# Performance work log

Measured on AMD Instinct MI355X. Metric: run time of the kernel, lower is better.

The kernel has to match this reference:

```python
import jax, jax.numpy as jnp
import numpy as np

B, S, DIM, H, D = 4, 2048, 1024, 16, 64
WINDOW = 512  # max_mem_segments * window_size


def _rotary_angles(seq_len, dim_head):
    inv_freq = 1.0 / (10000.0 ** (jnp.arange(0, dim_head, 2, dtype=jnp.float32) / dim_head))
    freqs = jnp.arange(seq_len, dtype=jnp.float32)[:, None] * inv_freq[None, :]  # [S, D/2]
    return jnp.repeat(freqs, 2, axis=-1)  # [S, D] interleaved


def _rotate_half(x):
    x1 = x[..., 0::2]
    x2 = x[..., 1::2]
    return jnp.stack((-x2, x1), axis=-1).reshape(x.shape)


def _apply_rotary(x, angles):
    # x: [b h n d], angles: [n d]
    return x * jnp.cos(angles) + _rotate_half(x) * jnp.sin(angles)


def setup_inputs() -> dict:
    key = jax.random.key(0)
    ks = jax.random.split(key, 7)
    tokens = jax.random.normal(ks[0], (B, S, DIM), dtype=jnp.float32)
    value_residual = jax.random.normal(ks[1], (B, H, S, D), dtype=jnp.float32)
    s = 0.02
    Wq = jax.random.normal(ks[2], (DIM, H * D), dtype=jnp.float32) * s
    Wkv = jax.random.normal(ks[3], (DIM, 2 * H * D), dtype=jnp.float32) * s
    Wout = jax.random.normal(ks[4], (H * D, DIM), dtype=jnp.float32) * s
    Wgate = jax.random.normal(ks[5], (DIM, H), dtype=jnp.float32) * s
    Wmix = jax.random.normal(ks[6], (DIM, H), dtype=jnp.float32) * s
    return {"tokens": tokens, "value_residual": value_residual, "Wq": Wq,
            "Wkv": Wkv, "Wout": Wout, "Wgate": Wgate, "Wmix": Wmix}


def reference(tokens, value_residual, Wq, Wkv, Wout, Wgate, Wmix):
    b, n, dim = tokens.shape
    scale = D ** -0.5

    def split_heads(t):  # [b n (h d)] -> [b h n d]
        return t.reshape(b, n, H, D).transpose(0, 2, 1, 3)

    q = split_heads(tokens @ Wq)
    kv = tokens @ Wkv
    k = split_heads(kv[..., : H * D])
    v = split_heads(kv[..., H * D:])

    q = q * scale

    # value-residual lerp: v.lerp(value_residual, mix)
    mix = jax.nn.sigmoid(jnp.einsum('bnd,dh->bhn', tokens, Wmix))[..., None]  # [b h n 1]
    v = v + (value_residual - v) * mix

    angles = _rotary_angles(n, D)
    q = _apply_rotary(q, angles)
    k = _apply_rotary(k, angles)

    sim = jnp.einsum('bhid,bhjd->bhij', q, k)

    # fixed-window causal mask: dist = i - j; masked if dist < 0 or dist > WINDOW
    pos = jnp.arange(n)
    dist = pos[:, None] - pos[None, :]
    mask = (dist < 0) | (dist > WINDOW)
    neg = -jnp.finfo(sim.dtype).max
    sim = jnp.where(mask[None, None], neg, sim)

    attn = jax.nn.softmax(sim, axis=-1)
    out = jnp.einsum('bhij,bhjd->bhid', attn, v)

    gates = jax.nn.sigmoid(jnp.einsum('bnd,dh->bhn', tokens, Wgate))[..., None]  # [b h n 1]
    out = out * gates

    out = out.transpose(0, 2, 1, 3).reshape(b, n, H * D)
    return out @ Wout
```

## Files before the change

### kernel.cpp

```cpp
#include <hip/hip_runtime.h>

#define NH 16
#define SLEN 2048
#define DMODEL 1024
#define DHEAD 64
#define WIN 512
#define NB 4

typedef unsigned short u16;
typedef unsigned int u32;
typedef unsigned long long u64;
typedef __attribute__((ext_vector_type(8))) __bf16 bf16x8;
typedef __attribute__((ext_vector_type(4))) float floatx4;

__device__ __forceinline__ float b2f(u32 bits16) {
  union { u32 i; float f; } x; x.i = bits16 << 16; return x.f;
}
__device__ __forceinline__ u16 f2b(float f) {
  union { float f; u32 i; } x; x.f = f;
  u32 r = x.i + 0x7fffu + ((x.i >> 16) & 1u);
  return (u16)(r >> 16);
}

__device__ __forceinline__ void gl2lds16(const u16* g, u16* l) {
  __builtin_amdgcn_global_load_lds(
      (const __attribute__((address_space(1))) unsigned int*)g,
      (__attribute__((address_space(3))) unsigned int*)l, 16, 0, 0);
}

__global__ __launch_bounds__(256) void prep_all(
    const float* __restrict__ tokens, const float* __restrict__ Wq,
    const float* __restrict__ Wkv, const float* __restrict__ Wout,
    const float* __restrict__ Wmix, const float* __restrict__ Wgate,
    u64* __restrict__ tokA64, u16* __restrict__ WqkvT, u16* __restrict__ WoutT,
    u16* __restrict__ Wmg, float2* __restrict__ rtab) {
  __shared__ u16 T[64][72];
  const int blk = blockIdx.x, tid = threadIdx.x;
  if (blk < 8192) {
    int i = blk * 256 + tid;
    float4 f = reinterpret_cast<const float4*>(tokens)[i];
    union { u16 u[4]; u64 ll; } pk;
    pk.u[0] = f2b(f.x); pk.u[1] = f2b(f.y); pk.u[2] = f2b(f.z); pk.u[3] = f2b(f.w);
    tokA64[i] = pk.ll;
  } else if (blk < 9216) {
    const float* src; u16* dst; int ld, nb, n0, k0;
    if (blk < 8960) {
      int tile = blk - 8192;
      n0 = (tile % 48) * 64; k0 = (tile / 48) * 64;
      if (n0 < 1024) { src = Wq; ld = 1024; nb = n0; }
      else { src = Wkv; ld = 2048; nb = n0 - 1024; }
      dst = WqkvT;
    } else {
      int tile = blk - 8960;
      n0 = (tile % 16) * 64; k0 = (tile / 16) * 64;
      src = Wout; ld = 1024; nb = n0; dst = WoutT;
    }
#pragma unroll
    for (int i = 0; i < 16; ++i) {
      int e = i * 256 + tid;
      int kr = e >> 6, nc = e & 63;
      T[kr][nc] = f2b(src[(size_t)(k0 + kr) * ld + nb + nc]);
    }
    __syncthreads();
#pragma unroll
    for (int i = 0; i < 16; ++i) {
      int e = i * 256 + tid;
      int nr = e >> 6, kc = e & 63;
      dst[(size_t)(n0 + nr) * 1024 + k0 + kc] = T[kc][nr];
    }
  } else if (blk < 9344) {
    int idx = (blk - 9216) * 256 + tid;
    int n = idx >> 10, k = idx & 1023;
    float v = (n < 16) ? Wmix[k * 16 + n] : Wgate[k * 16 + (n - 16)];
    Wmg[idx] = f2b(v);
  } else {
    int idx = (blk - 9344) * 256 + tid;
    int s = idx >> 5, t = idx & 31;
    float inv = __expf((float)t * -0.2878231366f);
    float ang = (float)s * inv;
    float sn, cs;
    __sincosf(ang, &sn, &cs);
    rtab[idx] = make_float2(cs, sn);
  }
}

__global__ __launch_bounds__(256) void mixgate_mfma(const u16* __restrict__ A,
    const u16* __restrict__ Wmg, float* __restrict__ mixws, float* __restrict__ gatews) {
  const int lane = threadIdx.x & 63, w = threadIdx.x >> 6;
  const int lm = lane & 15, quad = lane >> 4;
  const int row0 = (blockIdx.x * 4 + w) * 32;

  floatx4 acc[2][2];
#pragma unroll
  for (int i = 0; i < 2; ++i)
#pragma unroll
    for (int j = 0; j < 2; ++j)
      acc[i][j] = (floatx4){0.f, 0.f, 0.f, 0.f};

#pragma unroll 4
  for (int k0 = 0; k0 < 1024; k0 += 32) {
    bf16x8 af[2], bf[2];
#pragma unroll
    for (int mt = 0; mt < 2; ++mt)
      af[mt] = *reinterpret_cast<const bf16x8*>(
          &A[(size_t)(row0 + mt * 16 + lm) * 1024 + k0 + quad * 8]);
#pragma unroll
    for (int nt = 0; nt < 2; ++nt)
      bf[nt] = *reinterpret_cast<const bf16x8*>(
          &Wmg[(size_t)(nt * 16 + lm) * 1024 + k0 + quad * 8]);
#pragma unroll
    for (int mt = 0; mt < 2; ++mt)
#pragma unroll
      for (int nt = 0; nt < 2; ++nt)
        acc[mt][nt] = __builtin_amdgcn_mfma_f32_16x16x32_bf16(af[mt], bf[nt], acc[mt][nt], 0, 0, 0);
  }

#pragma unroll
  for (int mt = 0; mt < 2; ++mt)
#pragma unroll
    for (int r = 0; r < 4; ++r) {
      int grow = row0 + mt * 16 + quad * 4 + r;
      int b = grow >> 11, s = grow & 2047;
#pragma unroll
      for (int nt = 0; nt < 2; ++nt) {
        int n = nt * 16 + lm;
        float sig = 1.0f / (1.0f + __expf(-acc[mt][nt][r]));
        int h = n & 15;
        (n < 16 ? mixws : gatews)[(b * NH + h) * SLEN + s] = sig;
      }
    }
}

template<int MODE>
__global__ __launch_bounds__(256, 3) void gemm_bf16_bt(
    const u16* __restrict__ A, const u16* __restrict__ Bt,
    float* __restrict__ C,
    u16* __restrict__ qws, u16* __restrict__ kws, u16* __restrict__ vws,
    const float* __restrict__ vres, const float* __restrict__ mixws,
    const float2* __restrict__ rtab,
    int M, int N, int K) {
  __shared__ u16 smem[16384];
  u16* As = smem;
  u16* Bs = smem + 8192;
  const int tid = threadIdx.x;
  const int row0 = blockIdx.y * 128, col0 = blockIdx.x * 128;
  const int w = tid >> 6, lane = tid & 63;
  const int wr = (w >> 1) * 64, wc = (w & 1) * 64;
  const int lm = lane & 15, quad = lane >> 4;

  floatx4 acc[4][4];
#pragma unroll
  for (int i = 0; i < 4; ++i)
#pragma unroll
    for (int j = 0; j < 4; ++j)
      acc[i][j] = (floatx4){0.f, 0.f, 0.f, 0.f};

  for (int k0 = 0; k0 < K; k0 += 64) {
#pragma unroll
    for (int i = 0; i < 4; ++i) {
      int slot = i * 256 + tid;
      int r = slot >> 3, cc = slot & 7;
      int csrc = (cc ^ (r & 7)) * 8;
      gl2lds16(&A[(size_t)(row0 + r) * K + k0 + csrc], As + slot * 8);
      gl2lds16(&Bt[(size_t)(col0 + r) * K + k0 + csrc], Bs + slot * 8);
    }
    __syncthreads();
#pragma unroll
    for (int j = 0; j < 2; ++j) {
      bf16x8 af[4], bfr[4];
#pragma unroll
      for (int mt = 0; mt < 4; ++mt) {
        int ra = wr + mt * 16 + lm;
        af[mt] = *reinterpret_cast<const bf16x8*>(As + (ra * 8 + ((j * 4 + quad) ^ (ra & 7))) * 8);
      }
#pragma unroll
      for (int nt = 0; nt < 4; ++nt) {
        int rb = wc + nt * 16 + lm;
        bfr[nt] = *reinterpret_cast<const bf16x8*>(Bs + (rb * 8 + ((j * 4 + quad) ^ (rb & 7))) * 8);
      }
#pragma unroll
      for (int mt = 0; mt < 4; ++mt)
#pragma unroll
        for (int nt = 0; nt < 4; ++nt)
          acc[mt][nt] = __builtin_amdgcn_mfma_f32_16x16x32_bf16(af[mt], bfr[nt], acc[mt][nt], 0, 0, 0);
    }
    __syncthreads();
  }

  if (MODE == 0) {
#pragma unroll
    for (int mt = 0; mt < 4; ++mt)
#pragma unroll
      for (int r = 0; r < 4; ++r) {
        int grow = row0 + wr + mt * 16 + quad * 4 + r;
#pragma unroll
        for (int nt = 0; nt < 4; ++nt)
          C[(size_t)grow * N + col0 + wc + nt * 16 + lm] = acc[mt][nt][r];
      }
  } else {
    const int seg = col0 >> 10;
    const int b = row0 >> 11, s0 = row0 & 2047;
    if (seg < 2) {
      u16* dst = seg ? kws : qws;
      const float qs = seg ? 1.0f : 0.125f;
#pragma unroll
      for (int mt = 0; mt < 4; ++mt)
#pragma unroll
        for (int r = 0; r < 4; ++r) {
          int s = s0 + wr + mt * 16 + quad * 4 + r;
#pragma unroll
          for (int nt = 0; nt < 4; ++nt) {
            int nn = ((col0 + wc) & 1023) + nt * 16 + lm;
            int h = nn >> 6, d = nn & 63;
            float val = acc[mt][nt][r] * qs;
            float2 cs = rtab[(s << 5) + (d >> 1)];
            float partner = __shfl_xor(val, 1);
            float o = (d & 1) ? fmaf(val, cs.x, partner * cs.y)
                              : fmaf(val, cs.x, -partner * cs.y);
            dst[((size_t)((b * NH + h) * SLEN + s)) * 64 + d] = f2b(o);
          }
        }
    } else {
      const int h0 = (col0 - 2048) >> 6;
      u16 (*Vt)[136] = (u16(*)[136])smem;
#pragma unroll
      for (int p = 0; p < 2; ++p) {
        const int bh = b * NH + h0 + p;
        __syncthreads();
        if ((w & 1) == p) {
#pragma unroll
          for (int mt = 0; mt < 4; ++mt)
#pragma unroll
            for (int nt = 0; nt < 4; ++nt) {
              const int d = nt * 16 + lm;
              const int sl = wr + mt * 16 + quad * 4;
              union { u16 u[4]; u64 ll; } pk;
#pragma unroll
              for (int r = 0; r < 4; ++r) {
                int s = s0 + sl + r;
                float val = acc[mt][nt][r];
                float mv = mixws[bh * SLEN + s];
                float o = val + (vres[((size_t)(bh * SLEN + s)) * 64 + d] - val) * mv;
                pk.u[r] = f2b(o);
              }
              *reinterpret_cast<u64*>(&Vt[d][sl]) = pk.ll;
            }
        }
        __syncthreads();
        const int drow = tid >> 2, chunk = tid & 3;
        const u16* src = &Vt[drow][chunk * 32];
        u16* dst = vws + ((size_t)(bh * 64 + drow)) * SLEN + s0 + chunk * 32;
#pragma unroll
        for (int j = 0; j < 4; ++j)
          reinterpret_cast<uint4*>(dst)[j] = reinterpret_cast<const uint4*>(src)[j];
      }
    }
  }
}

__global__ __launch_bounds__(256) void attn_mfma_kernel(
    const u16* __restrict__ q, const u16* __restrict__ k, const u16* __restrict__ vt,
    const float* __restrict__ gate, u16* __restrict__ X) {
  __shared__ u16 Ks[4096];
  __shared__ u16 Vs[4096];
  __shared__ u16 Ps[4][16][72];
  const int tid = threadIdx.x;
  const int w = tid >> 6, lane = tid & 63;
  const int lm = lane & 15, quad = lane >> 4;
  const int blk = blockIdx.x;
  const int qt = blk & 31;
  const int h = (blk >> 5) & 15;
  const int b = blk >> 9;
  const int bh = b * NH + h;
  const int q0 = qt * 64;
  const size_t kqbase = (size_t)bh * SLEN * 64;
  const size_t vbase  = (size_t)bh * 64 * SLEN;

  bf16x8 qf[2];
  {
    const u16* qrow = q + kqbase + (size_t)(q0 + w * 16 + lm) * 64;
    qf[0] = *reinterpret_cast<const bf16x8*>(qrow + quad * 8);
    qf[1] = *reinterpret_cast<const bf16x8*>(qrow + 32 + quad * 8);
  }

  floatx4 o[4];
#pragma unroll
  for (int nt = 0; nt < 4; ++nt) o[nt] = (floatx4){0.f, 0.f, 0.f, 0.f};
  float lsum = 0.f;
  const int iq = q0 + w * 16 + lm;

  const int c_first = (q0 >= WIN) ? ((q0 - WIN) >> 6) : 0;
  const int c_last = q0 >> 6;
  const int vrow = tid >> 3, vcol = (tid & 7) * 8;
  for (int c = c_first; c <= c_last; ++c) {
    const int c0 = c << 6;
    __syncthreads();
    {
      const u16* kg = k + kqbase + (size_t)c0 * 64;
      gl2lds16(kg + tid * 8, Ks + tid * 8);
      gl2lds16(kg + 2048 + tid * 8, Ks + 2048 + tid * 8);
      const u16* vg = vt + vbase + c0;
      gl2lds16(vg + (size_t)vrow * SLEN + vcol, Vs + tid * 8);
      gl2lds16(vg + (size_t)(vrow + 32) * SLEN + vcol, Vs + 2048 + tid * 8);
    }
    __syncthreads();

    floatx4 st[4];
#pragma unroll
    for (int mt = 0; mt < 4; ++mt) {
      bf16x8 kf0 = *reinterpret_cast<const bf16x8*>(&Ks[(mt * 16 + lm) * 64 + quad * 8]);
      bf16x8 kf1 = *reinterpret_cast<const bf16x8*>(&Ks[(mt * 16 + lm) * 64 + 32 + quad * 8]);
      st[mt] = __builtin_amdgcn_mfma_f32_16x16x32_bf16(kf0, qf[0],
                   (floatx4){0.f, 0.f, 0.f, 0.f}, 0, 0, 0);
      st[mt] = __builtin_amdgcn_mfma_f32_16x16x32_bf16(kf1, qf[1], st[mt], 0, 0, 0);
    }
    const bool need_mask = (c == c_first && q0 >= WIN) || (c == c_last);
    if (need_mask) {
#pragma unroll
      for (int mt = 0; mt < 4; ++mt)
#pragma unroll
        for (int r = 0; r < 4; ++r) {
          int j = c0 + mt * 16 + quad * 4 + r;
          bool valid = (j <= iq) && (j >= iq - WIN);
          if (!valid) st[mt][r] = -3.0e38f;
        }
    }
    float p[4][4], psum = 0.f;
#pragma unroll
    for (int mt = 0; mt < 4; ++mt)
#pragma unroll
      for (int r = 0; r < 4; ++r) {
        p[mt][r] = __expf(st[mt][r]);
        psum += p[mt][r];
      }
    psum += __shfl_xor(psum, 16);
    psum += __shfl_xor(psum, 32);
    lsum += psum;
#pragma unroll
    for (int mt = 0; mt < 4; ++mt) {
      union { u16 u[4]; u64 ll; } pk;
#pragma unroll
      for (int r = 0; r < 4; ++r) pk.u[r] = f2b(p[mt][r]);
      *reinterpret_cast<u64*>(&Ps[w][lm][mt * 16 + quad * 4]) = pk.ll;
    }
    __builtin_amdgcn_wave_barrier();
    __builtin_amdgcn_s_waitcnt(0xC07F);
    __builtin_amdgcn_wave_barrier();
    bf16x8 af0 = *reinterpret_cast<const bf16x8*>(&Ps[w][lm][quad * 8]);
    bf16x8 af1 = *reinterpret_cast<const bf16x8*>(&Ps[w][lm][32 + quad * 8]);
#pragma unroll
    for (int nt = 0; nt < 4; ++nt) {
      bf16x8 vf0 = *reinterpret_cast<const bf16x8*>(&Vs[(nt * 16 + lm) * 64 + quad * 8]);
      bf16x8 vf1 = *reinterpret_cast<const bf16x8*>(&Vs[(nt * 16 + lm) * 64 + 32 + quad * 8]);
      o[nt] = __builtin_amdgcn_mfma_f32_16x16x32_bf16(af0, vf0, o[nt], 0, 0, 0);
      o[nt] = __builtin_amdgcn_mfma_f32_16x16x32_bf16(af1, vf1, o[nt], 0, 0, 0);
    }
  }
  float linv[4], g[4];
#pragma unroll
  for (int r = 0; r < 4; ++r) {
    linv[r] = 1.0f / __shfl(lsum, quad * 4 + r);
    g[r] = gate[bh * SLEN + q0 + w * 16 + quad * 4 + r];
  }
#pragma unroll
  for (int r = 0; r < 4; ++r) {
    int i = q0 + w * 16 + quad * 4 + r;
    u16* xrow = X + ((size_t)(b * SLEN + i)) * 1024 + h * 64;
#pragma unroll
    for (int nt = 0; nt < 4; ++nt)
      xrow[nt * 16 + lm] = f2b(o[nt][r] * linv[r] * g[r]);
  }
}

extern "C" void kernel_launch(void* const* d_in, const int* in_sizes, int n_in,
                              void* d_out, int out_size, void* d_ws, size_t ws_size,
                              hipStream_t stream) {
  (void)in_sizes; (void)n_in; (void)out_size; (void)ws_size;
  const float* tokens = (const float*)d_in[0];
  const float* vres   = (const float*)d_in[1];
  const float* Wq     = (const float*)d_in[2];
  const float* Wkv    = (const float*)d_in[3];
  const float* Wout   = (const float*)d_in[4];
  const float* Wgate  = (const float*)d_in[5];
  const float* Wmix   = (const float*)d_in[6];
  float* out = (float*)d_out;

  char* p = (char*)d_ws;
  auto alloc = [&](size_t bytes) { char* r = p; p += (bytes + 255) & ~(size_t)255; return r; };
  u16*  tokA   = (u16*)alloc(8192ull * 1024 * 2);
  u16*  WqkvT  = (u16*)alloc(3072ull * 1024 * 2);
  u16*  WoutT  = (u16*)alloc(1024ull * 1024 * 2);
  u16*  Wmg    = (u16*)alloc(32ull * 1024 * 2);
  float2* rtab = (float2*)alloc(65536ull * 8);
  u16*  qws    = (u16*)alloc(8388608ull * 2);
  u16*  kws    = (u16*)alloc(8388608ull * 2);
  u16*  vws    = (u16*)alloc(8388608ull * 2);
  u16*  Xws    = (u16*)alloc(8388608ull * 2);
  float* mixws = (float*)alloc(131072ull * 4);
  float* gatews= (float*)alloc(131072ull * 4);

  prep_all<<<9600, 256, 0, stream>>>(tokens, Wq, Wkv, Wout, Wmix, Wgate,
      (u64*)tokA, WqkvT, WoutT, Wmg, rtab);
  mixgate_mfma<<<64, 256, 0, stream>>>(tokA, Wmg, mixws, gatews);
  gemm_bf16_bt<1><<<dim3(24, 64), 256, 0, stream>>>(tokA, WqkvT, nullptr,
      qws, kws, vws, vres, mixws, rtab, 8192, 3072, 1024);
  attn_mfma_kernel<<<2048, 256, 0, stream>>>(qws, kws, vws, gatews, Xws);
  gemm_bf16_bt<0><<<dim3(8, 64), 256, 0, stream>>>(Xws, WoutT, out,
      nullptr, nullptr, nullptr, nullptr, nullptr, nullptr, 8192, 1024, 1024);
}
```

Before: 298.1 us.

## Rewrite GEMM as 256x128-tile triple-buffered pipeline with 512 threads and swizzled block order

Replaces the single-buffered 128x128 GEMM with a 256x128 tile computed by 512 threads. A three-stage LDS ring issues global-to-LDS loads two k-steps ahead, interleaved between MFMA halves, with explicit vmcnt waits, a single barrier per step, and s_setprio around the MFMA blocks. Work-group ids are remapped in groups of eight to improve L2 locality, and the V-transpose epilogue now handles both heads at once. The aim is to hide global load latency and cut barrier stalls, at the cost of much more LDS per block and lower occupancy.

```diff
diff --git a/kernel.cpp b/kernel.cpp
--- a/kernel.cpp
+++ b/kernel.cpp
@@ -132,21 +132,23 @@
 }
 
 template<int MODE>
-__global__ __launch_bounds__(256, 3) void gemm_bf16_bt(
+__global__ __launch_bounds__(512, 2) void gemm_pipe(
     const u16* __restrict__ A, const u16* __restrict__ Bt,
     float* __restrict__ C,
     u16* __restrict__ qws, u16* __restrict__ kws, u16* __restrict__ vws,
     const float* __restrict__ vres, const float* __restrict__ mixws,
-    const float2* __restrict__ rtab,
-    int M, int N, int K) {
-  __shared__ u16 smem[16384];
-  u16* As = smem;
-  u16* Bs = smem + 8192;
+    const float2* __restrict__ rtab, int N) {
+  __shared__ u16 smem[73728];
   const int tid = threadIdx.x;
-  const int row0 = blockIdx.y * 128, col0 = blockIdx.x * 128;
+  const int nbx = N >> 7;
+  const int wg = (blockIdx.x & 7) * (gridDim.x >> 3) + (blockIdx.x >> 3);
+  const int bx = wg % nbx, by = wg / nbx;
+  const int row0 = by * 256, col0 = bx * 128;
   const int w = tid >> 6, lane = tid & 63;
   const int wr = (w >> 1) * 64, wc = (w & 1) * 64;
   const int lm = lane & 15, quad = lane >> 4;
+  const int NT = 16;
+  const int sr = tid >> 3, sc = tid & 7;
 
   floatx4 acc[4][4];
 #pragma unroll
@@ -155,36 +157,116 @@
     for (int j = 0; j < 4; ++j)
       acc[i][j] = (floatx4){0.f, 0.f, 0.f, 0.f};
 
-  for (int k0 = 0; k0 < K; k0 += 64) {
-#pragma unroll
-    for (int i = 0; i < 4; ++i) {
-      int slot = i * 256 + tid;
-      int r = slot >> 3, cc = slot & 7;
-      int csrc = (cc ^ (r & 7)) * 8;
-      gl2lds16(&A[(size_t)(row0 + r) * K + k0 + csrc], As + slot * 8);
-      gl2lds16(&Bt[(size_t)(col0 + r) * K + k0 + csrc], Bs + slot * 8);
-    }
-    __syncthreads();
-#pragma unroll
-    for (int j = 0; j < 2; ++j) {
-      bf16x8 af[4], bfr[4];
-#pragma unroll
-      for (int mt = 0; mt < 4; ++mt) {
-        int ra = wr + mt * 16 + lm;
-        af[mt] = *reinterpret_cast<const bf16x8*>(As + (ra * 8 + ((j * 4 + quad) ^ (ra & 7))) * 8);
-      }
-#pragma unroll
-      for (int nt = 0; nt < 4; ++nt) {
-        int rb = wc + nt * 16 + lm;
-        bfr[nt] = *reinterpret_cast<const bf16x8*>(Bs + (rb * 8 + ((j * 4 + quad) ^ (rb & 7))) * 8);
-      }
-#pragma unroll
-      for (int mt = 0; mt < 4; ++mt)
-#pragma unroll
-        for (int nt = 0; nt < 4; ++nt)
-          acc[mt][nt] = __builtin_amdgcn_mfma_f32_16x16x32_bf16(af[mt], bfr[nt], acc[mt][nt], 0, 0, 0);
-    }
-    __syncthreads();
+#pragma unroll
+  for (int tt = 0; tt < 2; ++tt) {
+    u16* As = smem + tt * 24576;
+    u16* Bs = As + 16384;
+    const int k0 = tt * 64;
+#pragma unroll
+    for (int la = 0; la < 4; ++la) {
+      int r = la * 64 + sr;
+      gl2lds16(&A[(size_t)(row0 + r) * 1024 + k0 + ((sc ^ (r & 7)) << 3)],
+               As + (((r << 3) + sc) << 3));
+    }
+#pragma unroll
+    for (int lb = 0; lb < 2; ++lb) {
+      int r = lb * 64 + sr;
+      gl2lds16(&Bt[(size_t)(col0 + r) * 1024 + k0 + ((sc ^ (r & 7)) << 3)],
+               Bs + (((r << 3) + sc) << 3));
+    }
+  }
+
+  int cur = 0;
+  for (int t = 0; t < NT; ++t) {
+    u16* As = smem + cur * 24576;
+    u16* Bs = As + 16384;
+    if (t < NT - 1) { asm volatile("s_waitcnt vmcnt(6)" ::: "memory"); }
+    else           { asm volatile("s_waitcnt vmcnt(0)" ::: "memory"); }
+    __builtin_amdgcn_s_barrier();
+    asm volatile("" ::: "memory");
+
+    int sidx = cur + 2; if (sidx >= 3) sidx -= 3;
+    u16* Sa = smem + sidx * 24576;
+    u16* Sb = Sa + 16384;
+    const int ks = (t + 2) << 6;
+    const bool do_stage = (t + 2) < NT;
+
+    if (do_stage) {
+#pragma unroll
+      for (int la = 0; la < 2; ++la) {
+        int r = la * 64 + sr;
+        gl2lds16(&A[(size_t)(row0 + r) * 1024 + ks + ((sc ^ (r & 7)) << 3)],
+                 Sa + (((r << 3) + sc) << 3));
+      }
+      {
+        int r = sr;
+        gl2lds16(&Bt[(size_t)(col0 + r) * 1024 + ks + ((sc ^ (r & 7)) << 3)],
+                 Sb + (((r << 3) + sc) << 3));
+      }
+    }
+    bf16x8 bfr[4][2];
+#pragma unroll
+    for (int nt = 0; nt < 4; ++nt) {
+      int rb = wc + nt * 16 + lm;
+#pragma unroll
+      for (int j = 0; j < 2; ++j)
+        bfr[nt][j] = *reinterpret_cast<const bf16x8*>(
+            Bs + (((rb << 3) + (((j << 2) + quad) ^ (rb & 7))) << 3));
+    }
+    bf16x8 af0[2][2];
+#pragma unroll
+    for (int mh = 0; mh < 2; ++mh) {
+      int ra = wr + mh * 16 + lm;
+#pragma unroll
+      for (int j = 0; j < 2; ++j)
+        af0[mh][j] = *reinterpret_cast<const bf16x8*>(
+            As + (((ra << 3) + (((j << 2) + quad) ^ (ra & 7))) << 3));
+    }
+    __builtin_amdgcn_s_setprio(1);
+#pragma unroll
+    for (int mh = 0; mh < 2; ++mh)
+#pragma unroll
+      for (int nt = 0; nt < 4; ++nt)
+#pragma unroll
+        for (int j = 0; j < 2; ++j)
+          acc[mh][nt] = __builtin_amdgcn_mfma_f32_16x16x32_bf16(
+              af0[mh][j], bfr[nt][j], acc[mh][nt], 0, 0, 0);
+    __builtin_amdgcn_s_setprio(0);
+
+    if (do_stage) {
+#pragma unroll
+      for (int la = 2; la < 4; ++la) {
+        int r = la * 64 + sr;
+        gl2lds16(&A[(size_t)(row0 + r) * 1024 + ks + ((sc ^ (r & 7)) << 3)],
+                 Sa + (((r << 3) + sc) << 3));
+      }
+      {
+        int r = 64 + sr;
+        gl2lds16(&Bt[(size_t)(col0 + r) * 1024 + ks + ((sc ^ (r & 7)) << 3)],
+                 Sb + (((r << 3) + sc) << 3));
+      }
+    }
+    bf16x8 af1[2][2];
+#pragma unroll
+    for (int mh = 0; mh < 2; ++mh) {
+      int ra = wr + (2 + mh) * 16 + lm;
+#pragma unroll
+      for (int j = 0; j < 2; ++j)
+        af1[mh][j] = *reinterpret_cast<const bf16x8*>(
+            As + (((ra << 3) + (((j << 2) + quad) ^ (ra & 7))) << 3));
+    }
+    __builtin_amdgcn_s_setprio(1);
+#pragma unroll
+    for (int mh = 0; mh < 2; ++mh)
+#pragma unroll
+      for (int nt = 0; nt < 4; ++nt)
+#pragma unroll
+        for (int j = 0; j < 2; ++j)
+          acc[2 + mh][nt] = __builtin_amdgcn_mfma_f32_16x16x32_bf16(
+              af1[mh][j], bfr[nt][j], acc[2 + mh][nt], 0, 0, 0);
+    __builtin_amdgcn_s_setprio(0);
+
+    cur += 1; if (cur >= 3) cur -= 3;
   }
 
   if (MODE == 0) {
@@ -199,18 +281,19 @@
       }
   } else {
     const int seg = col0 >> 10;
-    const int b = row0 >> 11, s0 = row0 & 2047;
     if (seg < 2) {
       u16* dst = seg ? kws : qws;
       const float qs = seg ? 1.0f : 0.125f;
+      const int colb = (col0 & 1023) + wc;
 #pragma unroll
       for (int mt = 0; mt < 4; ++mt)
 #pragma unroll
         for (int r = 0; r < 4; ++r) {
-          int s = s0 + wr + mt * 16 + quad * 4 + r;
+          int sg = row0 + wr + mt * 16 + quad * 4 + r;
+          int b = sg >> 11, s = sg & 2047;
 #pragma unroll
           for (int nt = 0; nt < 4; ++nt) {
-            int nn = ((col0 + wc) & 1023) + nt * 16 + lm;
+            int nn = colb + nt * 16 + lm;
             int h = nn >> 6, d = nn & 63;
             float val = acc[mt][nt][r] * qs;
             float2 cs = rtab[(s << 5) + (d >> 1)];
@@ -222,37 +305,37 @@
         }
     } else {
       const int h0 = (col0 - 2048) >> 6;
-      u16 (*Vt)[136] = (u16(*)[136])smem;
-#pragma unroll
-      for (int p = 0; p < 2; ++p) {
-        const int bh = b * NH + h0 + p;
-        __syncthreads();
-        if ((w & 1) == p) {
-#pragma unroll
-          for (int mt = 0; mt < 4; ++mt)
-#pragma unroll
-            for (int nt = 0; nt < 4; ++nt) {
-              const int d = nt * 16 + lm;
-              const int sl = wr + mt * 16 + quad * 4;
-              union { u16 u[4]; u64 ll; } pk;
-#pragma unroll
-              for (int r = 0; r < 4; ++r) {
-                int s = s0 + sl + r;
-                float val = acc[mt][nt][r];
-                float mv = mixws[bh * SLEN + s];
-                float o = val + (vres[((size_t)(bh * SLEN + s)) * 64 + d] - val) * mv;
-                pk.u[r] = f2b(o);
-              }
-              *reinterpret_cast<u64*>(&Vt[d][sl]) = pk.ll;
-            }
+      const int p = (w & 1);
+      const int b = row0 >> 11, s0 = row0 & 2047;
+      const int bh = b * NH + h0 + p;
+      u16 (*Vt)[264] = reinterpret_cast<u16(*)[264]>(smem + p * 16896);
+      __syncthreads();
+#pragma unroll
+      for (int mt = 0; mt < 4; ++mt)
+#pragma unroll
+        for (int nt = 0; nt < 4; ++nt) {
+          const int d = nt * 16 + lm;
+          const int sl = wr + mt * 16 + quad * 4;
+          union { u16 u[4]; u64 ll; } pk;
+#pragma unroll
+          for (int r = 0; r < 4; ++r) {
+            int s = s0 + sl + r;
+            float val = acc[mt][nt][r];
+            float mv = mixws[bh * SLEN + s];
+            float o = val + (vres[((size_t)(bh * SLEN + s)) * 64 + d] - val) * mv;
+            pk.u[r] = f2b(o);
+          }
+          *reinterpret_cast<u64*>(&Vt[d][sl]) = pk.ll;
         }
-        __syncthreads();
-        const int drow = tid >> 2, chunk = tid & 3;
-        const u16* src = &Vt[drow][chunk * 32];
-        u16* dst = vws + ((size_t)(bh * 64 + drow)) * SLEN + s0 + chunk * 32;
-#pragma unroll
-        for (int j = 0; j < 4; ++j)
-          reinterpret_cast<uint4*>(dst)[j] = reinterpret_cast<const uint4*>(src)[j];
+      __syncthreads();
+#pragma unroll
+      for (int it = 0; it < 8; ++it) {
+        int idx = it * 512 + tid;
+        int ph = idx >> 11, rem = idx & 2047;
+        int d = rem >> 5, ch = rem & 31;
+        const u16* src = smem + ph * 16896 + d * 264 + ch * 8;
+        u16* dst = vws + ((size_t)((b * NH + h0 + ph) * 64 + d)) * SLEN + s0 + ch * 8;
+        *reinterpret_cast<uint4*>(dst) = *reinterpret_cast<const uint4*>(src);
       }
     }
   }
@@ -402,9 +485,9 @@
   prep_all<<<9600, 256, 0, stream>>>(tokens, Wq, Wkv, Wout, Wmix, Wgate,
       (u64*)tokA, WqkvT, WoutT, Wmg, rtab);
   mixgate_mfma<<<64, 256, 0, stream>>>(tokA, Wmg, mixws, gatews);
-  gemm_bf16_bt<1><<<dim3(24, 64), 256, 0, stream>>>(tokA, WqkvT, nullptr,
-      qws, kws, vws, vres, mixws, rtab, 8192, 3072, 1024);
+  gemm_pipe<1><<<768, 512, 0, stream>>>(tokA, WqkvT, nullptr,
+      qws, kws, vws, vres, mixws, rtab, 3072);
   attn_mfma_kernel<<<2048, 256, 0, stream>>>(qws, kws, vws, gatews, Xws);
-  gemm_bf16_bt<0><<<dim3(8, 64), 256, 0, stream>>>(Xws, WoutT, out,
-      nullptr, nullptr, nullptr, nullptr, nullptr, nullptr, 8192, 1024, 1024);
-}
+  gemm_pipe<0><<<256, 512, 0, stream>>>(Xws, WoutT, out,
+      nullptr, nullptr, nullptr, nullptr, nullptr, nullptr, 1024);
+}
```

New measurement: 286.0 us. 4.1% less time.

## Replace projection GEMMs with triple-buffered 256x128 pipelined kernel and swizzled grid

Applied to the files above, without the earlier changes.

Both projection GEMMs move to a new kernel with 512-thread blocks computing 256x128 tiles. It triple-buffers LDS stages so global-to-LDS loads run two K-steps ahead of the MFMA work, using explicit vmcnt waits, raw ds_read_b128 with immediate offsets, and setprio around the MFMA bursts. The grid is remapped into an XCD-friendly order to improve L2 reuse. The epilogue is adjusted for the taller tile, including a single-pass V transpose through LDS. The cost is much larger LDS use and hard-coded K=1024 and wait counts.

```diff
diff --git a/kernel.cpp b/kernel.cpp
--- a/kernel.cpp
+++ b/kernel.cpp
@@ -27,6 +27,20 @@
       (const __attribute__((address_space(1))) unsigned int*)g,
       (__attribute__((address_space(3))) unsigned int*)l, 16, 0, 0);
 }
+
+template<int OFF>
+__device__ __forceinline__ bf16x8 ldsr128(u32 addr) {
+  bf16x8 r;
+  if constexpr (OFF == 0)
+    asm volatile("ds_read_b128 %0, %1" : "=v"(r) : "v"(addr));
+  else
+    asm volatile("ds_read_b128 %0, %1 offset:%2" : "=v"(r) : "v"(addr), "i"(OFF));
+  return r;
+}
+
+#define WAIT_VM6  asm volatile("s_waitcnt vmcnt(6)" ::: "memory")
+#define WAIT_VM0  asm volatile("s_waitcnt vmcnt(0)" ::: "memory")
+#define WAIT_LGKM0 asm volatile("s_waitcnt lgkmcnt(0)" ::: "memory")
 
 __global__ __launch_bounds__(256) void prep_all(
     const float* __restrict__ tokens, const float* __restrict__ Wq,
@@ -132,21 +146,35 @@
 }
 
 template<int MODE>
-__global__ __launch_bounds__(256, 3) void gemm_bf16_bt(
+__global__ __launch_bounds__(512, 2) void gemm_pipe(
     const u16* __restrict__ A, const u16* __restrict__ Bt,
     float* __restrict__ C,
     u16* __restrict__ qws, u16* __restrict__ kws, u16* __restrict__ vws,
     const float* __restrict__ vres, const float* __restrict__ mixws,
-    const float2* __restrict__ rtab,
-    int M, int N, int K) {
-  __shared__ u16 smem[16384];
-  u16* As = smem;
-  u16* Bs = smem + 8192;
+    const float2* __restrict__ rtab, int N) {
+  __shared__ u16 smem[73728];
   const int tid = threadIdx.x;
-  const int row0 = blockIdx.y * 128, col0 = blockIdx.x * 128;
+  const int nbx = N >> 7;
+  const int wg = (blockIdx.x & 7) * (gridDim.x >> 3) + (blockIdx.x >> 3);
+  const int bx = wg % nbx, by = wg / nbx;
+  const int row0 = by * 256, col0 = bx * 128;
   const int w = tid >> 6, lane = tid & 63;
   const int wr = (w >> 1) * 64, wc = (w & 1) * 64;
   const int lm = lane & 15, quad = lane >> 4;
+  const int NT = 16;
+  const int sr = tid >> 3, sc = tid & 7;
+  const int sl0 = (sr * 8 + sc) * 8;
+  const u16* gA = A + (size_t)(row0 + sr) * 1024 + ((sc ^ (sr & 7)) << 3);
+  const u16* gB = Bt + (size_t)(col0 + sr) * 1024 + ((sc ^ (sr & 7)) << 3);
+
+  const u32 ldsbase = (u32)(size_t)(__attribute__((address_space(3))) u16*)smem;
+  u32 arow[2], brow[2];
+#pragma unroll
+  for (int j = 0; j < 2; ++j) {
+    u32 cslot = (u32)((j * 4 + quad) ^ (lm & 7));
+    arow[j] = (u32)(wr + lm) * 128 + cslot * 16;
+    brow[j] = (u32)(wc + lm) * 128 + cslot * 16;
+  }
 
   floatx4 acc[4][4];
 #pragma unroll
@@ -155,36 +183,67 @@
     for (int j = 0; j < 4; ++j)
       acc[i][j] = (floatx4){0.f, 0.f, 0.f, 0.f};
 
-  for (int k0 = 0; k0 < K; k0 += 64) {
-#pragma unroll
-    for (int i = 0; i < 4; ++i) {
-      int slot = i * 256 + tid;
-      int r = slot >> 3, cc = slot & 7;
-      int csrc = (cc ^ (r & 7)) * 8;
-      gl2lds16(&A[(size_t)(row0 + r) * K + k0 + csrc], As + slot * 8);
-      gl2lds16(&Bt[(size_t)(col0 + r) * K + k0 + csrc], Bs + slot * 8);
-    }
-    __syncthreads();
+  auto stage3 = [&](u16* Sa, u16* Sb, int ks, int half) {
+    if (half == 0) {
+      gl2lds16(gA + ks, Sa + sl0);
+      gl2lds16(gA + 65536 + ks, Sa + 4096 + sl0);
+      gl2lds16(gB + ks, Sb + sl0);
+    } else {
+      gl2lds16(gA + 131072 + ks, Sa + 8192 + sl0);
+      gl2lds16(gA + 196608 + ks, Sa + 12288 + sl0);
+      gl2lds16(gB + 65536 + ks, Sb + 4096 + sl0);
+    }
+  };
+
+#pragma unroll
+  for (int tt = 0; tt < 2; ++tt) {
+    u16* Sa = smem + tt * 24576;
+    u16* Sb = Sa + 16384;
+    stage3(Sa, Sb, tt * 64, 0);
+    stage3(Sa, Sb, tt * 64, 1);
+  }
+
+  int cur = 0;
+  for (int t = 0; t < NT; ++t) {
+    int sidx = cur + 2; if (sidx >= 3) sidx -= 3;
+    u16* Sa = smem + sidx * 24576;
+    u16* Sb = Sa + 16384;
+    const int ks = (t + 2) << 6;
+    const bool do_stage = t < NT - 2;
+    const u32 abase = ldsbase + (u32)cur * 49152u;
+
+    if (t < NT - 1) { WAIT_VM6; } else { WAIT_VM0; }
+    __builtin_amdgcn_s_barrier();
+
 #pragma unroll
     for (int j = 0; j < 2; ++j) {
+      u32 aaddr = abase + arow[j];
+      u32 baddr = abase + 32768u + brow[j];
       bf16x8 af[4], bfr[4];
-#pragma unroll
-      for (int mt = 0; mt < 4; ++mt) {
-        int ra = wr + mt * 16 + lm;
-        af[mt] = *reinterpret_cast<const bf16x8*>(As + (ra * 8 + ((j * 4 + quad) ^ (ra & 7))) * 8);
-      }
-#pragma unroll
-      for (int nt = 0; nt < 4; ++nt) {
-        int rb = wc + nt * 16 + lm;
-        bfr[nt] = *reinterpret_cast<const bf16x8*>(Bs + (rb * 8 + ((j * 4 + quad) ^ (rb & 7))) * 8);
-      }
+      af[0] = ldsr128<0>(aaddr);
+      af[1] = ldsr128<2048>(aaddr);
+      af[2] = ldsr128<4096>(aaddr);
+      af[3] = ldsr128<6144>(aaddr);
+      bfr[0] = ldsr128<0>(baddr);
+      bfr[1] = ldsr128<2048>(baddr);
+      bfr[2] = ldsr128<4096>(baddr);
+      bfr[3] = ldsr128<6144>(baddr);
+      if (do_stage) stage3(Sa, Sb, ks, j);
+      __builtin_amdgcn_sched_barrier(0);
+      __builtin_amdgcn_s_barrier();
+      WAIT_LGKM0;
+      __builtin_amdgcn_sched_barrier(0);
+      __builtin_amdgcn_s_setprio(1);
 #pragma unroll
       for (int mt = 0; mt < 4; ++mt)
 #pragma unroll
         for (int nt = 0; nt < 4; ++nt)
-          acc[mt][nt] = __builtin_amdgcn_mfma_f32_16x16x32_bf16(af[mt], bfr[nt], acc[mt][nt], 0, 0, 0);
-    }
-    __syncthreads();
+          acc[mt][nt] = __builtin_amdgcn_mfma_f32_16x16x32_bf16(
+              af[mt], bfr[nt], acc[mt][nt], 0, 0, 0);
+      __builtin_amdgcn_s_setprio(0);
+    }
+
+    cur += 1; if (cur >= 3) cur -= 3;
   }
 
   if (MODE == 0) {
@@ -199,18 +258,19 @@
       }
   } else {
     const int seg = col0 >> 10;
-    const int b = row0 >> 11, s0 = row0 & 2047;
     if (seg < 2) {
       u16* dst = seg ? kws : qws;
       const float qs = seg ? 1.0f : 0.125f;
+      const int colb = (col0 & 1023) + wc;
 #pragma unroll
       for (int mt = 0; mt < 4; ++mt)
 #pragma unroll
         for (int r = 0; r < 4; ++r) {
-          int s = s0 + wr + mt * 16 + quad * 4 + r;
+          int sg = row0 + wr + mt * 16 + quad * 4 + r;
+          int b = sg >> 11, s = sg & 2047;
 #pragma unroll
           for (int nt = 0; nt < 4; ++nt) {
-            int nn = ((col0 + wc) & 1023) + nt * 16 + lm;
+            int nn = colb + nt * 16 + lm;
             int h = nn >> 6, d = nn & 63;
             float val = acc[mt][nt][r] * qs;
             float2 cs = rtab[(s << 5) + (d >> 1)];
@@ -222,37 +282,37 @@
         }
     } else {
       const int h0 = (col0 - 2048) >> 6;
-      u16 (*Vt)[136] = (u16(*)[136])smem;
-#pragma unroll
-      for (int p = 0; p < 2; ++p) {
-        const int bh = b * NH + h0 + p;
-        __syncthreads();
-        if ((w & 1) == p) {
-#pragma unroll
-          for (int mt = 0; mt < 4; ++mt)
-#pragma unroll
-            for (int nt = 0; nt < 4; ++nt) {
-              const int d = nt * 16 + lm;
-              const int sl = wr + mt * 16 + quad * 4;
-              union { u16 u[4]; u64 ll; } pk;
-#pragma unroll
-              for (int r = 0; r < 4; ++r) {
-                int s = s0 + sl + r;
-                float val = acc[mt][nt][r];
-                float mv = mixws[bh * SLEN + s];
-                float o = val + (vres[((size_t)(bh * SLEN + s)) * 64 + d] - val) * mv;
-                pk.u[r] = f2b(o);
-              }
-              *reinterpret_cast<u64*>(&Vt[d][sl]) = pk.ll;
-            }
+      const int p = (w & 1);
+      const int b = row0 >> 11, s0 = row0 & 2047;
+      const int bh = b * NH + h0 + p;
+      u16 (*Vt)[264] = reinterpret_cast<u16(*)[264]>(smem + p * 16896);
+      __syncthreads();
+#pragma unroll
+      for (int mt = 0; mt < 4; ++mt)
+#pragma unroll
+        for (int nt = 0; nt < 4; ++nt) {
+          const int d = nt * 16 + lm;
+          const int sl = wr + mt * 16 + quad * 4;
+          union { u16 u[4]; u64 ll; } pk;
+#pragma unroll
+          for (int r = 0; r < 4; ++r) {
+            int s = s0 + sl + r;
+            float val = acc[mt][nt][r];
+            float mv = mixws[bh * SLEN + s];
+            float o = val + (vres[((size_t)(bh * SLEN + s)) * 64 + d] - val) * mv;
+            pk.u[r] = f2b(o);
+          }
+          *reinterpret_cast<u64*>(&Vt[d][sl]) = pk.ll;
         }
-        __syncthreads();
-        const int drow = tid >> 2, chunk = tid & 3;
-        const u16* src = &Vt[drow][chunk * 32];
-        u16* dst = vws + ((size_t)(bh * 64 + drow)) * SLEN + s0 + chunk * 32;
-#pragma unroll
-        for (int j = 0; j < 4; ++j)
-          reinterpret_cast<uint4*>(dst)[j] = reinterpret_cast<const uint4*>(src)[j];
+      __syncthreads();
+#pragma unroll
+      for (int it = 0; it < 8; ++it) {
+        int idx = it * 512 + tid;
+        int ph = idx >> 11, rem = idx & 2047;
+        int d = rem >> 5, ch = rem & 31;
+        const u16* src = smem + ph * 16896 + d * 264 + ch * 8;
+        u16* dst = vws + ((size_t)((b * NH + h0 + ph) * 64 + d)) * SLEN + s0 + ch * 8;
+        *reinterpret_cast<uint4*>(dst) = *reinterpret_cast<const uint4*>(src);
       }
     }
   }
@@ -402,9 +462,9 @@
   prep_all<<<9600, 256, 0, stream>>>(tokens, Wq, Wkv, Wout, Wmix, Wgate,
       (u64*)tokA, WqkvT, WoutT, Wmg, rtab);
   mixgate_mfma<<<64, 256, 0, stream>>>(tokA, Wmg, mixws, gatews);
-  gemm_bf16_bt<1><<<dim3(24, 64), 256, 0, stream>>>(tokA, WqkvT, nullptr,
-      qws, kws, vws, vres, mixws, rtab, 8192, 3072, 1024);
+  gemm_pipe<1><<<768, 512, 0, stream>>>(tokA, WqkvT, nullptr,
+      qws, kws, vws, vres, mixws, rtab, 3072);
   attn_mfma_kernel<<<2048, 256, 0, stream>>>(qws, kws, vws, gatews, Xws);
-  gemm_bf16_bt<0><<<dim3(8, 64), 256, 0, stream>>>(Xws, WoutT, out,
-      nullptr, nullptr, nullptr, nullptr, nullptr, nullptr, 8192, 1024, 1024);
-}
+  gemm_pipe<0><<<256, 512, 0, stream>>>(Xws, WoutT, out,
+      nullptr, nullptr, nullptr, nullptr, nullptr, nullptr, 1024);
+}
```

Result: faster. 284.3 us (-4.6%).
